# Optimization experiments

Measured on AMD Instinct MI355X. Metric: run time of the kernel, lower is better.

The kernel has to match this reference:

```python
import jax, jax.numpy as jnp
import numpy as np
import math

HEADS = 8
DIM_HEAD = 64
EMB = 512
GROUPS = 32
EPS = 100000.0  # module's literal default norm_eps


def setup_inputs() -> dict:
    key = jax.random.key(0)
    ks = jax.random.split(key, 11)
    B, D, H, W = 2, EMB, 64, 64
    s = 1.0 / math.sqrt(EMB)
    inp = {
        "input": jax.random.normal(ks[0], (B, D, H, W), dtype=jnp.float32),
        "gn_gamma": jnp.ones((EMB,), dtype=jnp.float32),
        "gn_beta": jnp.zeros((EMB,), dtype=jnp.float32),
        "wq": jax.random.normal(ks[1], (EMB, EMB), dtype=jnp.float32) * s,
        "bq": jax.random.normal(ks[2], (EMB,), dtype=jnp.float32) * 0.01,
        "wk": jax.random.normal(ks[3], (EMB, EMB), dtype=jnp.float32) * s,
        "bk": jax.random.normal(ks[4], (EMB,), dtype=jnp.float32) * 0.01,
        "wv": jax.random.normal(ks[5], (EMB, EMB), dtype=jnp.float32) * s,
        "bv": jax.random.normal(ks[6], (EMB,), dtype=jnp.float32) * 0.01,
        "wo": jax.random.normal(ks[7], (EMB, EMB), dtype=jnp.float32) * s,
        "bo": jax.random.normal(ks[8], (EMB,), dtype=jnp.float32) * 0.01,
    }
    return inp


def reference(input, gn_gamma, gn_beta, wq, bq, wk, bk, wv, bv, wo, bo):
    B, D, H, W = input.shape
    S = H * W
    residual = input

    # GroupNorm(32, D) over (C/G, H, W) per group, affine per-channel
    xg = input.reshape(B, GROUPS, (D // GROUPS) * H * W)
    mu = jnp.mean(xg, axis=-1, keepdims=True)
    var = jnp.var(xg, axis=-1, keepdims=True)
    xn = (xg - mu) / jnp.sqrt(var + EPS)
    xn = xn.reshape(B, D, H, W) * gn_gamma[:, None, None] + gn_beta[:, None, None]

    # (B, D, H, W) -> (B, S, D)
    x = xn.reshape(B, D, S).transpose(0, 2, 1)

    # projections (torch Linear: y = x @ W.T + b)
    q = (x @ wq.T + bq).reshape(B, S, HEADS, DIM_HEAD).transpose(0, 2, 1, 3)
    k = (x @ wk.T + bk).reshape(B, S, HEADS, DIM_HEAD).transpose(0, 2, 1, 3)
    v = (x @ wv.T + bv).reshape(B, S, HEADS, DIM_HEAD).transpose(0, 2, 1, 3)

    scale = 1.0 / math.sqrt(DIM_HEAD)
    scores = jnp.einsum("bhqd,bhkd->bhqk", q * scale, k)  # [B, h, S, S]
    attn = jax.nn.softmax(scores, axis=-1)
    o = jnp.einsum("bhqk,bhkd->bhqd", attn, v)  # [B, h, S, dh]
    o = o.transpose(0, 2, 1, 3).reshape(B, S, D)

    out = o @ wo.T + bo  # [B, S, D]
    out = out.transpose(0, 2, 1).reshape(B, D, H, W)
    return out + residual
```

## Files before the change

kernel.cpp:

```cpp
#include <hip/hip_runtime.h>

#define EMB 512
#define SEQ 4096
#define BATCH 2
#define NH 8
#define DH 64
#define GN_EPS 100000.0f
#define ALPHA 0.125f

typedef __bf16 bf16;
typedef __bf16 bf16x8 __attribute__((ext_vector_type(8)));
typedef float f32x4 __attribute__((ext_vector_type(4)));

typedef __attribute__((address_space(1))) unsigned int u32g;
typedef __attribute__((address_space(3))) unsigned int u32l;
__device__ __forceinline__ void gll16(const void* g, void* l) {
  __builtin_amdgcn_global_load_lds((const u32g*)g, (u32l*)l, 16, 0, 0);
}

__device__ __forceinline__ void stage8(const bf16* g, size_t rowStride, bf16* lds, int lane) {
  const int r = lane >> 3, cc = (lane & 7) ^ r;
  gll16(g + (size_t)r * rowStride + cc * 8, lds + lane * 8);
}
__device__ __forceinline__ bf16x8 frag(const bf16* lds, int r, int cc) {
  return *(const bf16x8*)&lds[(((r << 3) + (cc ^ (r & 7))) << 3)];
}

__global__ __launch_bounds__(256) void stats_k(const float* __restrict__ in,
                                               float* __restrict__ rs,
                                               float* __restrict__ ss) {
  const int row = blockIdx.x;
  const float4* p = (const float4*)(in + (size_t)row * SEQ);
  float s = 0.f, s2 = 0.f;
#pragma unroll
  for (int i = 0; i < 4; ++i) {
    float4 v = p[i * 256 + threadIdx.x];
    s += v.x + v.y + v.z + v.w;
    s2 += v.x * v.x + v.y * v.y + v.z * v.z + v.w * v.w;
  }
#pragma unroll
  for (int o = 32; o > 0; o >>= 1) {
    s += __shfl_down(s, o, 64);
    s2 += __shfl_down(s2, o, 64);
  }
  __shared__ float red[8];
  const int wave = threadIdx.x >> 6, lane = threadIdx.x & 63;
  if (lane == 0) { red[wave] = s; red[4 + wave] = s2; }
  __syncthreads();
  if (threadIdx.x == 0) {
    rs[row] = red[0] + red[1] + red[2] + red[3];
    ss[row] = red[4] + red[5] + red[6] + red[7];
  }
}

__global__ __launch_bounds__(256) void prep_k(const float* __restrict__ wq, const float* __restrict__ wk,
                                              const float* __restrict__ wv, const float* __restrict__ wo,
                                              const float* __restrict__ bv,
                                              const float* __restrict__ rs, const float* __restrict__ ss,
                                              const float* __restrict__ gamma, const float* __restrict__ beta,
                                              bf16* __restrict__ wqt, bf16* __restrict__ wkb,
                                              bf16* __restrict__ wvb, bf16* __restrict__ wob,
                                              float* __restrict__ kxa, float* __restrict__ vsuma) {
  __shared__ float t[64][65];
  __shared__ float xs[1024];
  __shared__ float gmu[64], grs[64];
  const int y = blockIdx.y, tid = threadIdx.x;
  if (y < 8) {
    const int c0 = blockIdx.x * 64, r0 = y * 64;
#pragma unroll
    for (int p = 0; p < 16; ++p) {
      int lin = p * 256 + tid;
      int rl = lin >> 6, cl = lin & 63;
      t[rl][cl] = wq[(size_t)(r0 + rl) * EMB + c0 + cl];
    }
    __syncthreads();
#pragma unroll
    for (int p = 0; p < 16; ++p) {
      int lin = p * 256 + tid;
      int cl = lin >> 6, rl = lin & 63;
      wqt[(size_t)(c0 + cl) * EMB + r0 + rl] = (bf16)t[rl][cl];
    }
  } else {
    const int wi = y - 8;
    const float* W = wi == 0 ? wk : wi == 1 ? wv : wo;
    bf16* WO = wi == 0 ? wkb : wi == 1 ? wvb : wob;
    if (wi < 2) {
      if (tid < 64) {
        float s = 0.f, s2 = 0.f;
#pragma unroll
        for (int c = 0; c < 16; ++c) { s += rs[tid * 16 + c]; s2 += ss[tid * 16 + c]; }
        float mu = s * (1.f / 65536.f);
        float var = s2 * (1.f / 65536.f) - mu * mu;
        gmu[tid] = mu;
        grs[tid] = rsqrtf(var + GN_EPS);
      }
      __syncthreads();
      for (int idx = tid; idx < 1024; idx += 256) {
        int d = idx & 511;
        float s = grs[idx >> 4] * gamma[d];
        float tt = beta[d] - gmu[idx >> 4] * s;
        xs[idx] = s * rs[idx] + 4096.f * tt;
      }
      __syncthreads();
    }
    const int n = blockIdx.x * 64 + (tid >> 2);
    const float* Wr = W + (size_t)n * EMB;
    float dot0 = 0.f, dot1 = 0.f;
    const int dq = (tid & 3) * 128;
    for (int d = dq; d < dq + 128; d += 4) {
      float4 w4 = *(const float4*)&Wr[d];
      if (wi < 2) {
        float4 x0 = *(const float4*)&xs[d];
        float4 x1 = *(const float4*)&xs[EMB + d];
        dot0 += w4.x * x0.x + w4.y * x0.y + w4.z * x0.z + w4.w * x0.w;
        dot1 += w4.x * x1.x + w4.y * x1.y + w4.z * x1.z + w4.w * x1.w;
      }
      bf16 r[4] = {(bf16)w4.x, (bf16)w4.y, (bf16)w4.z, (bf16)w4.w};
      *(uint2*)&WO[(size_t)n * EMB + d] = *(uint2*)r;
    }
    if (wi < 2) {
      dot0 += __shfl_xor(dot0, 1, 4); dot0 += __shfl_xor(dot0, 2, 4);
      dot1 += __shfl_xor(dot1, 1, 4); dot1 += __shfl_xor(dot1, 2, 4);
      if ((tid & 3) == 0) {
        if (wi == 0) { kxa[n] = dot0; kxa[EMB + n] = dot1; }
        else { vsuma[n] = dot0 + 4096.f * bv[n]; vsuma[EMB + n] = dot1 + 4096.f * bv[n]; }
      }
    }
  }
}

__global__ __launch_bounds__(256) void nx_k(const float* __restrict__ in,
                                            const float* __restrict__ rs,
                                            const float* __restrict__ ss,
                                            const float* __restrict__ gamma,
                                            const float* __restrict__ beta,
                                            bf16* __restrict__ xds,
                                            bf16* __restrict__ xsd) {
  __shared__ float t[64][65];
  __shared__ float gmu4[4], grs4[4], scl[64], ttl[64];
  const int s0 = blockIdx.x * 64, d0 = blockIdx.y * 64, b = blockIdx.z;
  const int tid = threadIdx.x;
  if (tid < 4) {
    float s = 0.f, s2 = 0.f;
    int base = b * EMB + d0 + tid * 16;
#pragma unroll
    for (int c = 0; c < 16; ++c) { s += rs[base + c]; s2 += ss[base + c]; }
    float mu = s * (1.f / 65536.f);
    float var = s2 * (1.f / 65536.f) - mu * mu;
    gmu4[tid] = mu;
    grs4[tid] = rsqrtf(var + GN_EPS);
  }
  __syncthreads();
  if (tid < 64) {
    int d = d0 + tid;
    float s = grs4[tid >> 4] * gamma[d];
    scl[tid] = s;
    ttl[tid] = beta[d] - gmu4[tid >> 4] * s;
  }
  __syncthreads();
#pragma unroll
  for (int p = 0; p < 16; ++p) {
    int lin = p * 256 + tid;
    int dl = lin >> 6, sl = lin & 63;
    size_t idx = ((size_t)b * EMB + d0 + dl) * SEQ + s0 + sl;
    float v = in[idx] * scl[dl] + ttl[dl];
    t[dl][sl] = v;
    xds[idx] = (bf16)v;
  }
  __syncthreads();
#pragma unroll
  for (int p = 0; p < 16; ++p) {
    int lin = p * 256 + tid;
    int sl = lin >> 6, dl = lin & 63;
    xsd[((size_t)b * SEQ + s0 + sl) * EMB + d0 + dl] = (bf16)t[dl][sl];
  }
}

__global__ __launch_bounds__(256) void graw2_k(const bf16* __restrict__ xds,
                                               float* __restrict__ pG) {
  __shared__ __align__(16) bf16 As[64 * 64];
  __shared__ __align__(16) bf16 Bs[64 * 64];
  int ti = 0, rem = blockIdx.x;
  while (rem >= 8 - ti) { rem -= 8 - ti; ++ti; }
  const int i0 = ti * 64, j0 = (ti + rem) * 64;
  const int kc = blockIdx.y, b = blockIdx.z;
  const bf16* X = xds + (size_t)b * EMB * SEQ;
  const int tid = threadIdx.x;
  const int wave = tid >> 6, lane = tid & 63, l16 = lane & 15, quad = lane >> 4;
  f32x4 acc[4] = {};
  for (int k0 = kc * 512; k0 < kc * 512 + 512; k0 += 64) {
#pragma unroll
    for (int p = 0; p < 2; ++p) {
      int g = wave * 2 + p;
      stage8(&X[(size_t)(i0 + g * 8) * SEQ + k0], SEQ, &As[g * 512], lane);
      stage8(&X[(size_t)(j0 + g * 8) * SEQ + k0], SEQ, &Bs[g * 512], lane);
    }
    __syncthreads();
#pragma unroll
    for (int kt = 0; kt < 2; ++kt) {
      bf16x8 af = frag(As, wave * 16 + l16, kt * 4 + quad);
#pragma unroll
      for (int nt = 0; nt < 4; ++nt) {
        bf16x8 bb = frag(Bs, nt * 16 + l16, kt * 4 + quad);
        acc[nt] = __builtin_amdgcn_mfma_f32_16x16x32_bf16(af, bb, acc[nt], 0, 0, 0);
      }
    }
    __syncthreads();
  }
  float* pg = pG + ((size_t)(b * 8 + kc) * 36 + blockIdx.x) * 4096;
#pragma unroll
  for (int nt = 0; nt < 4; ++nt)
#pragma unroll
    for (int r = 0; r < 4; ++r)
      pg[(wave * 16 + quad * 4 + r) * 64 + nt * 16 + l16] = acc[nt][r];
}

__global__ __launch_bounds__(256) void gsum_k(const float* __restrict__ pG,
                                              bf16* __restrict__ G) {
  const int b = blockIdx.x >> 10;
  const int e = ((blockIdx.x & 1023) << 8) + threadIdx.x;
  const int i = e >> 9, j = e & 511;
  int ti = i >> 6, tj = j >> 6, row = i & 63, col = j & 63;
  if (ti > tj) { int tmp = ti; ti = tj; tj = tmp; tmp = row; row = col; col = tmp; }
  const int tile = ti * 8 - (ti * (ti - 1)) / 2 + (tj - ti);
  const float* p = pG + (size_t)b * 8 * 36 * 4096 + (size_t)tile * 4096 + row * 64 + col;
  float s = 0.f;
#pragma unroll
  for (int kc = 0; kc < 8; ++kc) s += p[(size_t)kc * 36 * 4096];
  G[(size_t)b * 262144 + e] = (bf16)s;
}

__global__ __launch_bounds__(256) void t2pt_k(const bf16* __restrict__ wkb,
                                              const bf16* __restrict__ G,
                                              const bf16* __restrict__ wvb,
                                              float* __restrict__ pPt) {
  __shared__ __align__(16) bf16 As[64 * 64];
  __shared__ __align__(16) bf16 Bs[64 * 64];
  __shared__ __align__(16) bf16 Ps[4 * 16 * 72];
  const int n0 = blockIdx.x * 64, h = blockIdx.y, b = blockIdx.z;
  const int bh = b * NH + h;
  const int tid = threadIdx.x;
  const int wave = tid >> 6, lane = tid & 63, l16 = lane & 15, quad = lane >> 4;
  bf16* Pw = &Ps[wave * 16 * 72];
  f32x4 acc[4] = {};
  for (int k0 = 0; k0 < EMB; k0 += 64) {
#pragma unroll
    for (int p = 0; p < 2; ++p) {
      int g = wave * 2 + p;
      stage8(&wkb[(size_t)(h * DH + g * 8) * EMB + k0], EMB, &As[g * 512], lane);
      stage8(&G[((size_t)b * EMB + n0 + g * 8) * EMB + k0], EMB, &Bs[g * 512], lane);
    }
    __syncthreads();
#pragma unroll
    for (int kt = 0; kt < 2; ++kt) {
      bf16x8 af = frag(As, wave * 16 + l16, kt * 4 + quad);
#pragma unroll
      for (int nt = 0; nt < 4; ++nt) {
        bf16x8 bb = frag(Bs, nt * 16 + l16, kt * 4 + quad);
        acc[nt] = __builtin_amdgcn_mfma_f32_16x16x32_bf16(af, bb, acc[nt], 0, 0, 0);
      }
    }
    __syncthreads();
  }
#pragma unroll
  for (int nt = 0; nt < 4; ++nt)
#pragma unroll
    for (int r = 0; r < 4; ++r)
      Pw[(quad * 4 + r) * 72 + nt * 16 + l16] = (bf16)acc[nt][r];
#pragma unroll
  for (int p = 0; p < 2; ++p) {
    int g = wave * 2 + p;
    stage8(&wvb[(size_t)(h * DH + g * 8) * EMB + n0], EMB, &Bs[g * 512], lane);
  }
  __syncthreads();
  f32x4 accP[4] = {};
#pragma unroll
  for (int kt = 0; kt < 2; ++kt) {
    bf16x8 pf = *(const bf16x8*)&Pw[l16 * 72 + kt * 32 + quad * 8];
#pragma unroll
    for (int nt = 0; nt < 4; ++nt) {
      bf16x8 bb = frag(Bs, nt * 16 + l16, kt * 4 + quad);
      accP[nt] = __builtin_amdgcn_mfma_f32_16x16x32_bf16(pf, bb, accP[nt], 0, 0, 0);
    }
  }
  float* pp = pPt + ((size_t)bh * 8 + blockIdx.x) * 4096;
#pragma unroll
  for (int nt = 0; nt < 4; ++nt)
#pragma unroll
    for (int r = 0; r < 4; ++r)
      pp[(wave * 16 + quad * 4 + r) * 64 + nt * 16 + l16] = accP[nt][r];
}

__global__ __launch_bounds__(256) void ptsum_k(const float* __restrict__ pPt,
                                               const float* __restrict__ bk,
                                               const float* __restrict__ bv,
                                               const float* __restrict__ kxa,
                                               const float* __restrict__ vsuma,
                                               bf16* __restrict__ Pt) {
  const int bh = blockIdx.x;
  const int b = bh >> 3, h = bh & 7;
  const float sfac = ALPHA / 4096.f;
  for (int e = threadIdx.x; e < 4096; e += 256) {
    int kd = e >> 6, vd = e & 63;
    const float* p = pPt + (size_t)bh * 8 * 4096 + e;
    float s = 0.f;
#pragma unroll
    for (int nt = 0; nt < 8; ++nt) s += p[nt * 4096];
    float bvv = bv[h * DH + vd];
    float bkv = bk[h * DH + kd];
    float vx = vsuma[b * EMB + h * DH + vd] - 4096.f * bvv;
    float val = s + kxa[b * EMB + h * DH + kd] * bvv + bkv * vx + 4096.f * bkv * bvv;
    Pt[(size_t)bh * 4096 + e] = (bf16)(val * sfac);
  }
}

__global__ __launch_bounds__(256) void fchain_k(const bf16* __restrict__ wob,
                                                const bf16* __restrict__ Pt,
                                                const bf16* __restrict__ wqt,
                                                const float* __restrict__ wo,
                                                const float* __restrict__ bo,
                                                const float* __restrict__ bq,
                                                const float* __restrict__ vsuma,
                                                bf16* __restrict__ F,
                                                float* __restrict__ cst) {
  __shared__ __align__(16) bf16 Awo[64 * 64];
  __shared__ __align__(16) bf16 Bp[64 * 64];
  __shared__ __align__(16) bf16 Bwq[64 * 64];
  __shared__ __align__(16) bf16 Ps[4 * 16 * 72];
  __shared__ float yc[512];
  const int i0 = blockIdx.x * 64, j0 = blockIdx.y * 64, b = blockIdx.z;
  const int tid = threadIdx.x;
  const int wave = tid >> 6, lane = tid & 63, l16 = lane & 15, quad = lane >> 4;
  bf16* Pw = &Ps[wave * 16 * 72];
  f32x4 accF[4] = {};
  for (int h = 0; h < NH; ++h) {
    __syncthreads();
#pragma unroll
    for (int p = 0; p < 2; ++p) {
      int g = wave * 2 + p;
      stage8(&wob[(size_t)(i0 + g * 8) * EMB + h * DH], EMB, &Awo[g * 512], lane);
      stage8(&Pt[((size_t)(b * NH + h) * DH + g * 8) * DH], DH, &Bp[g * 512], lane);
      stage8(&wqt[(size_t)(j0 + g * 8) * EMB + h * DH], EMB, &Bwq[g * 512], lane);
    }
    __syncthreads();
    f32x4 at[4] = {};
#pragma unroll
    for (int kt = 0; kt < 2; ++kt) {
      bf16x8 af = frag(Awo, wave * 16 + l16, kt * 4 + quad);
#pragma unroll
      for (int nt = 0; nt < 4; ++nt) {
        bf16x8 bb = frag(Bp, nt * 16 + l16, kt * 4 + quad);
        at[nt] = __builtin_amdgcn_mfma_f32_16x16x32_bf16(af, bb, at[nt], 0, 0, 0);
      }
    }
#pragma unroll
    for (int nt = 0; nt < 4; ++nt)
#pragma unroll
      for (int r = 0; r < 4; ++r)
        Pw[(quad * 4 + r) * 72 + nt * 16 + l16] = (bf16)at[nt][r];
#pragma unroll
    for (int kt = 0; kt < 2; ++kt) {
      bf16x8 pf = *(const bf16x8*)&Pw[l16 * 72 + kt * 32 + quad * 8];
#pragma unroll
      for (int nt = 0; nt < 4; ++nt) {
        bf16x8 bb = frag(Bwq, nt * 16 + l16, kt * 4 + quad);
        accF[nt] = __builtin_amdgcn_mfma_f32_16x16x32_bf16(pf, bb, accF[nt], 0, 0, 0);
      }
    }
  }
#pragma unroll
  for (int nt = 0; nt < 4; ++nt)
#pragma unroll
    for (int r = 0; r < 4; ++r)
      F[((size_t)b * EMB + i0 + wave * 16 + quad * 4 + r) * EMB + j0 + nt * 16 + l16] =
          (bf16)accF[nt][r];
  if (j0 == 0) {
    __syncthreads();
    for (int e = tid; e < 512; e += 256) {
      int h = e >> 6, vd = e & 63;
      const bf16* pp = &Pt[(size_t)(b * NH + h) * DH * DH + vd];
      const float* bqh = &bq[h * DH];
      float a = 0.f;
#pragma unroll 8
      for (int kd = 0; kd < 64; ++kd) a += (float)pp[kd * DH] * bqh[kd];
      yc[e] = vsuma[b * EMB + e] * (1.f / 4096.f) + a;
    }
    __syncthreads();
    const int row = i0 + (tid >> 2);
    const float* wr = &wo[(size_t)row * EMB + (tid & 3) * 128];
    const float* yq = &yc[(tid & 3) * 128];
    float a = 0.f;
    for (int e = 0; e < 128; e += 4) {
      float4 w4 = *(const float4*)&wr[e];
      a += w4.x * yq[e] + w4.y * yq[e + 1] + w4.z * yq[e + 2] + w4.w * yq[e + 3];
    }
    a += __shfl_xor(a, 1, 4);
    a += __shfl_xor(a, 2, 4);
    if ((tid & 3) == 0) cst[b * EMB + row] = bo[row] + a;
  }
}

__global__ __launch_bounds__(256) void final_k(const bf16* __restrict__ F,
                                               const bf16* __restrict__ xsd,
                                               const float* __restrict__ cst,
                                               const float* __restrict__ in,
                                               float* __restrict__ out) {
  __shared__ __align__(16) bf16 As[128 * 64];
  __shared__ __align__(16) bf16 Bs[64 * 64];
  const int m0 = blockIdx.x * 128, s0 = blockIdx.y * 64, b = blockIdx.z;
  const bf16* Fb = F + (size_t)b * EMB * EMB;
  const bf16* Xb = xsd + (size_t)b * SEQ * EMB;
  const int tid = threadIdx.x;
  const int wave = tid >> 6, lane = tid & 63, l16 = lane & 15, quad = lane >> 4;
  f32x4 acc[2][4] = {};
  for (int k0 = 0; k0 < EMB; k0 += 64) {
#pragma unroll
    for (int p = 0; p < 4; ++p) {
      int g = wave * 4 + p;
      stage8(&Fb[(size_t)(m0 + g * 8) * EMB + k0], EMB, &As[g * 512], lane);
    }
#pragma unroll
    for (int p = 0; p < 2; ++p) {
      int g = wave * 2 + p;
      stage8(&Xb[(size_t)(s0 + g * 8) * EMB + k0], EMB, &Bs[g * 512], lane);
    }
    __syncthreads();
#pragma unroll
    for (int kt = 0; kt < 2; ++kt) {
      bf16x8 a0 = frag(As, wave * 32 + l16, kt * 4 + quad);
      bf16x8 a1 = frag(As, wave * 32 + 16 + l16, kt * 4 + quad);
#pragma unroll
      for (int nt = 0; nt < 4; ++nt) {
        bf16x8 bb = frag(Bs, nt * 16 + l16, kt * 4 + quad);
        acc[0][nt] = __builtin_amdgcn_mfma_f32_16x16x32_bf16(a0, bb, acc[0][nt], 0, 0, 0);
        acc[1][nt] = __builtin_amdgcn_mfma_f32_16x16x32_bf16(a1, bb, acc[1][nt], 0, 0, 0);
      }
    }
    __syncthreads();
  }
#pragma unroll
  for (int mt = 0; mt < 2; ++mt) {
    int rowl = m0 + wave * 32 + mt * 16 + quad * 4;
#pragma unroll
    for (int r = 0; r < 4; ++r) {
      float cv = cst[b * EMB + rowl + r];
      size_t base = ((size_t)b * EMB + rowl + r) * SEQ + s0;
#pragma unroll
      for (int nt = 0; nt < 4; ++nt) {
        size_t idx = base + nt * 16 + l16;
        out[idx] = in[idx] + cv + acc[mt][nt][r];
      }
    }
  }
}

extern "C" void kernel_launch(void* const* d_in, const int* in_sizes, int n_in,
                              void* d_out, int out_size, void* d_ws, size_t ws_size,
                              hipStream_t stream) {
  const float* inp = (const float*)d_in[0];
  const float* gam = (const float*)d_in[1];
  const float* bet = (const float*)d_in[2];
  const float* wq = (const float*)d_in[3];
  const float* bq = (const float*)d_in[4];
  const float* wk = (const float*)d_in[5];
  const float* bk = (const float*)d_in[6];
  const float* wv = (const float*)d_in[7];
  const float* bv = (const float*)d_in[8];
  const float* wo = (const float*)d_in[9];
  const float* bo = (const float*)d_in[10];
  float* out = (float*)d_out;
  (void)in_sizes; (void)n_in; (void)out_size; (void)ws_size;

  char* ws = (char*)d_ws;
  size_t off = 0;
  auto take = [&](size_t bytes) -> char* {
    char* p = ws + off;
    off += (bytes + 255) & ~(size_t)255;
    return p;
  };
  float* rs = (float*)take(1024 * 4);
  float* ssq = (float*)take(1024 * 4);
  float* kxa = (float*)take(1024 * 4);
  float* vsuma = (float*)take(1024 * 4);
  float* cst = (float*)take(1024 * 4);
  const size_t WB = (size_t)EMB * EMB * sizeof(bf16);
  bf16* wkb = (bf16*)take(WB);
  bf16* wvb = (bf16*)take(WB);
  bf16* wob = (bf16*)take(WB);
  bf16* wqtb = (bf16*)take(WB);
  const size_t XB = (size_t)BATCH * SEQ * EMB * sizeof(bf16);
  bf16* xds = (bf16*)take(XB);
  bf16* xsd = (bf16*)take(XB);
  float* pG = (float*)take((size_t)BATCH * 8 * 36 * 4096 * sizeof(float));
  bf16* G = (bf16*)take((size_t)BATCH * EMB * EMB * sizeof(bf16));
  float* pPt = (float*)take((size_t)16 * 8 * 4096 * sizeof(float));
  bf16* Pt = (bf16*)take((size_t)16 * 4096 * sizeof(bf16));
  bf16* F = (bf16*)take((size_t)BATCH * EMB * EMB * sizeof(bf16));

  stats_k<<<1024, 256, 0, stream>>>(inp, rs, ssq);
  prep_k<<<dim3(8, 11), 256, 0, stream>>>(wq, wk, wv, wo, bv, rs, ssq, gam, bet,
                                          wqtb, wkb, wvb, wob, kxa, vsuma);
  nx_k<<<dim3(64, 8, 2), 256, 0, stream>>>(inp, rs, ssq, gam, bet, xds, xsd);
  graw2_k<<<dim3(36, 8, 2), 256, 0, stream>>>(xds, pG);
  gsum_k<<<2048, 256, 0, stream>>>(pG, G);
  t2pt_k<<<dim3(8, 8, 2), 256, 0, stream>>>(wkb, G, wvb, pPt);
  ptsum_k<<<16, 256, 0, stream>>>(pPt, bk, bv, kxa, vsuma, Pt);
  fchain_k<<<dim3(8, 8, 2), 256, 0, stream>>>(wob, Pt, wqtb, wo, bo, bq, vsuma, F, cst);
  final_k<<<dim3(4, 64, 2), 256, 0, stream>>>(F, xsd, cst, inp, out);
}
```

Before: 177.3 us.

## Fuse prep and normalize kernels, double split-K, split fchain into two GEMMs

Merges the weight-prep and normalize/transpose kernels into a single launch so their blocks run concurrently. It doubles the split-K factor in the Gram and t2pt GEMMs to put more blocks on the device, at the cost of larger partial buffers and reduction work. The serial per-head chain in fchain is split into a per-head Y kernel (with atomic accumulation of the constant term) and a plain GEMM. The bias-vector precompute moves into ptsum. This raises parallelism in the small late stages but adds one launch and an intermediate Y buffer round-trip.

```diff
diff --git a/kernel.cpp b/kernel.cpp
--- a/kernel.cpp
+++ b/kernel.cpp
@@ -53,126 +53,122 @@
   }
 }
 
-__global__ __launch_bounds__(256) void prep_k(const float* __restrict__ wq, const float* __restrict__ wk,
-                                              const float* __restrict__ wv, const float* __restrict__ wo,
-                                              const float* __restrict__ bv,
-                                              const float* __restrict__ rs, const float* __restrict__ ss,
-                                              const float* __restrict__ gamma, const float* __restrict__ beta,
-                                              bf16* __restrict__ wqt, bf16* __restrict__ wkb,
-                                              bf16* __restrict__ wvb, bf16* __restrict__ wob,
-                                              float* __restrict__ kxa, float* __restrict__ vsuma) {
+__global__ __launch_bounds__(256) void nxprep_k(const float* __restrict__ in,
+                                                const float* __restrict__ rs, const float* __restrict__ ss,
+                                                const float* __restrict__ gamma, const float* __restrict__ beta,
+                                                const float* __restrict__ wq, const float* __restrict__ wk,
+                                                const float* __restrict__ wv, const float* __restrict__ wo,
+                                                const float* __restrict__ bv,
+                                                bf16* __restrict__ xds, bf16* __restrict__ xsd,
+                                                bf16* __restrict__ wqt, bf16* __restrict__ wkb,
+                                                bf16* __restrict__ wvb, bf16* __restrict__ wob,
+                                                float* __restrict__ kxa, float* __restrict__ vsuma) {
   __shared__ float t[64][65];
   __shared__ float xs[1024];
   __shared__ float gmu[64], grs[64];
-  const int y = blockIdx.y, tid = threadIdx.x;
-  if (y < 8) {
-    const int c0 = blockIdx.x * 64, r0 = y * 64;
+  const int id = blockIdx.x, tid = threadIdx.x;
+  if (id < 1024) {
+    const int b = id >> 9, rem = id & 511;
+    const int d0 = (rem >> 6) * 64, s0 = (rem & 63) * 64;
+    if (tid < 4) {
+      float s = 0.f, s2 = 0.f;
+      int base = b * EMB + d0 + tid * 16;
+#pragma unroll
+      for (int c = 0; c < 16; ++c) { s += rs[base + c]; s2 += ss[base + c]; }
+      float mu = s * (1.f / 65536.f);
+      float var = s2 * (1.f / 65536.f) - mu * mu;
+      gmu[tid] = mu;
+      grs[tid] = rsqrtf(var + GN_EPS);
+    }
+    __syncthreads();
+    if (tid < 64) {
+      int d = d0 + tid;
+      float s = grs[tid >> 4] * gamma[d];
+      xs[tid] = s;
+      xs[64 + tid] = beta[d] - gmu[tid >> 4] * s;
+    }
+    __syncthreads();
 #pragma unroll
     for (int p = 0; p < 16; ++p) {
       int lin = p * 256 + tid;
-      int rl = lin >> 6, cl = lin & 63;
-      t[rl][cl] = wq[(size_t)(r0 + rl) * EMB + c0 + cl];
+      int dl = lin >> 6, sl = lin & 63;
+      size_t idx = ((size_t)b * EMB + d0 + dl) * SEQ + s0 + sl;
+      float v = in[idx] * xs[dl] + xs[64 + dl];
+      t[dl][sl] = v;
+      xds[idx] = (bf16)v;
     }
     __syncthreads();
 #pragma unroll
     for (int p = 0; p < 16; ++p) {
       int lin = p * 256 + tid;
-      int cl = lin >> 6, rl = lin & 63;
-      wqt[(size_t)(c0 + cl) * EMB + r0 + rl] = (bf16)t[rl][cl];
+      int sl = lin >> 6, dl = lin & 63;
+      xsd[((size_t)b * SEQ + s0 + sl) * EMB + d0 + dl] = (bf16)t[dl][sl];
     }
   } else {
-    const int wi = y - 8;
-    const float* W = wi == 0 ? wk : wi == 1 ? wv : wo;
-    bf16* WO = wi == 0 ? wkb : wi == 1 ? wvb : wob;
-    if (wi < 2) {
-      if (tid < 64) {
-        float s = 0.f, s2 = 0.f;
-#pragma unroll
-        for (int c = 0; c < 16; ++c) { s += rs[tid * 16 + c]; s2 += ss[tid * 16 + c]; }
-        float mu = s * (1.f / 65536.f);
-        float var = s2 * (1.f / 65536.f) - mu * mu;
-        gmu[tid] = mu;
-        grs[tid] = rsqrtf(var + GN_EPS);
+    const int r = id - 1024;
+    const int bx = r & 7, y = r >> 3;
+    if (y < 8) {
+      const int c0 = bx * 64, r0 = y * 64;
+#pragma unroll
+      for (int p = 0; p < 16; ++p) {
+        int lin = p * 256 + tid;
+        int rl = lin >> 6, cl = lin & 63;
+        t[rl][cl] = wq[(size_t)(r0 + rl) * EMB + c0 + cl];
       }
       __syncthreads();
-      for (int idx = tid; idx < 1024; idx += 256) {
-        int d = idx & 511;
-        float s = grs[idx >> 4] * gamma[d];
-        float tt = beta[d] - gmu[idx >> 4] * s;
-        xs[idx] = s * rs[idx] + 4096.f * tt;
-      }
-      __syncthreads();
-    }
-    const int n = blockIdx.x * 64 + (tid >> 2);
-    const float* Wr = W + (size_t)n * EMB;
-    float dot0 = 0.f, dot1 = 0.f;
-    const int dq = (tid & 3) * 128;
-    for (int d = dq; d < dq + 128; d += 4) {
-      float4 w4 = *(const float4*)&Wr[d];
+#pragma unroll
+      for (int p = 0; p < 16; ++p) {
+        int lin = p * 256 + tid;
+        int cl = lin >> 6, rl = lin & 63;
+        wqt[(size_t)(c0 + cl) * EMB + r0 + rl] = (bf16)t[rl][cl];
+      }
+    } else {
+      const int wi = y - 8;
+      const float* W = wi == 0 ? wk : wi == 1 ? wv : wo;
+      bf16* WO = wi == 0 ? wkb : wi == 1 ? wvb : wob;
       if (wi < 2) {
-        float4 x0 = *(const float4*)&xs[d];
-        float4 x1 = *(const float4*)&xs[EMB + d];
-        dot0 += w4.x * x0.x + w4.y * x0.y + w4.z * x0.z + w4.w * x0.w;
-        dot1 += w4.x * x1.x + w4.y * x1.y + w4.z * x1.z + w4.w * x1.w;
-      }
-      bf16 r[4] = {(bf16)w4.x, (bf16)w4.y, (bf16)w4.z, (bf16)w4.w};
-      *(uint2*)&WO[(size_t)n * EMB + d] = *(uint2*)r;
-    }
-    if (wi < 2) {
-      dot0 += __shfl_xor(dot0, 1, 4); dot0 += __shfl_xor(dot0, 2, 4);
-      dot1 += __shfl_xor(dot1, 1, 4); dot1 += __shfl_xor(dot1, 2, 4);
-      if ((tid & 3) == 0) {
-        if (wi == 0) { kxa[n] = dot0; kxa[EMB + n] = dot1; }
-        else { vsuma[n] = dot0 + 4096.f * bv[n]; vsuma[EMB + n] = dot1 + 4096.f * bv[n]; }
-      }
-    }
-  }
-}
-
-__global__ __launch_bounds__(256) void nx_k(const float* __restrict__ in,
-                                            const float* __restrict__ rs,
-                                            const float* __restrict__ ss,
-                                            const float* __restrict__ gamma,
-                                            const float* __restrict__ beta,
-                                            bf16* __restrict__ xds,
-                                            bf16* __restrict__ xsd) {
-  __shared__ float t[64][65];
-  __shared__ float gmu4[4], grs4[4], scl[64], ttl[64];
-  const int s0 = blockIdx.x * 64, d0 = blockIdx.y * 64, b = blockIdx.z;
-  const int tid = threadIdx.x;
-  if (tid < 4) {
-    float s = 0.f, s2 = 0.f;
-    int base = b * EMB + d0 + tid * 16;
-#pragma unroll
-    for (int c = 0; c < 16; ++c) { s += rs[base + c]; s2 += ss[base + c]; }
-    float mu = s * (1.f / 65536.f);
-    float var = s2 * (1.f / 65536.f) - mu * mu;
-    gmu4[tid] = mu;
-    grs4[tid] = rsqrtf(var + GN_EPS);
-  }
-  __syncthreads();
-  if (tid < 64) {
-    int d = d0 + tid;
-    float s = grs4[tid >> 4] * gamma[d];
-    scl[tid] = s;
-    ttl[tid] = beta[d] - gmu4[tid >> 4] * s;
-  }
-  __syncthreads();
-#pragma unroll
-  for (int p = 0; p < 16; ++p) {
-    int lin = p * 256 + tid;
-    int dl = lin >> 6, sl = lin & 63;
-    size_t idx = ((size_t)b * EMB + d0 + dl) * SEQ + s0 + sl;
-    float v = in[idx] * scl[dl] + ttl[dl];
-    t[dl][sl] = v;
-    xds[idx] = (bf16)v;
-  }
-  __syncthreads();
-#pragma unroll
-  for (int p = 0; p < 16; ++p) {
-    int lin = p * 256 + tid;
-    int sl = lin >> 6, dl = lin & 63;
-    xsd[((size_t)b * SEQ + s0 + sl) * EMB + d0 + dl] = (bf16)t[dl][sl];
+        if (tid < 64) {
+          float s = 0.f, s2 = 0.f;
+#pragma unroll
+          for (int c = 0; c < 16; ++c) { s += rs[tid * 16 + c]; s2 += ss[tid * 16 + c]; }
+          float mu = s * (1.f / 65536.f);
+          float var = s2 * (1.f / 65536.f) - mu * mu;
+          gmu[tid] = mu;
+          grs[tid] = rsqrtf(var + GN_EPS);
+        }
+        __syncthreads();
+        for (int idx = tid; idx < 1024; idx += 256) {
+          int d = idx & 511;
+          float s = grs[idx >> 4] * gamma[d];
+          float tt = beta[d] - gmu[idx >> 4] * s;
+          xs[idx] = s * rs[idx] + 4096.f * tt;
+        }
+        __syncthreads();
+      }
+      const int n = bx * 64 + (tid >> 2);
+      const float* Wr = W + (size_t)n * EMB;
+      float dot0 = 0.f, dot1 = 0.f;
+      const int dq = (tid & 3) * 128;
+      for (int d = dq; d < dq + 128; d += 4) {
+        float4 w4 = *(const float4*)&Wr[d];
+        if (wi < 2) {
+          float4 x0 = *(const float4*)&xs[d];
+          float4 x1 = *(const float4*)&xs[EMB + d];
+          dot0 += w4.x * x0.x + w4.y * x0.y + w4.z * x0.z + w4.w * x0.w;
+          dot1 += w4.x * x1.x + w4.y * x1.y + w4.z * x1.z + w4.w * x1.w;
+        }
+        bf16 rr[4] = {(bf16)w4.x, (bf16)w4.y, (bf16)w4.z, (bf16)w4.w};
+        *(uint2*)&WO[(size_t)n * EMB + d] = *(uint2*)rr;
+      }
+      if (wi < 2) {
+        dot0 += __shfl_xor(dot0, 1, 4); dot0 += __shfl_xor(dot0, 2, 4);
+        dot1 += __shfl_xor(dot1, 1, 4); dot1 += __shfl_xor(dot1, 2, 4);
+        if ((tid & 3) == 0) {
+          if (wi == 0) { kxa[n] = dot0; kxa[EMB + n] = dot1; }
+          else { vsuma[n] = dot0 + 4096.f * bv[n]; vsuma[EMB + n] = dot1 + 4096.f * bv[n]; }
+        }
+      }
+    }
   }
 }
 
@@ -188,7 +184,7 @@
   const int tid = threadIdx.x;
   const int wave = tid >> 6, lane = tid & 63, l16 = lane & 15, quad = lane >> 4;
   f32x4 acc[4] = {};
-  for (int k0 = kc * 512; k0 < kc * 512 + 512; k0 += 64) {
+  for (int k0 = kc * 256; k0 < kc * 256 + 256; k0 += 64) {
 #pragma unroll
     for (int p = 0; p < 2; ++p) {
       int g = wave * 2 + p;
@@ -207,7 +203,7 @@
     }
     __syncthreads();
   }
-  float* pg = pG + ((size_t)(b * 8 + kc) * 36 + blockIdx.x) * 4096;
+  float* pg = pG + ((size_t)(b * 16 + kc) * 36 + blockIdx.x) * 4096;
 #pragma unroll
   for (int nt = 0; nt < 4; ++nt)
 #pragma unroll
@@ -223,10 +219,10 @@
   int ti = i >> 6, tj = j >> 6, row = i & 63, col = j & 63;
   if (ti > tj) { int tmp = ti; ti = tj; tj = tmp; tmp = row; row = col; col = tmp; }
   const int tile = ti * 8 - (ti * (ti - 1)) / 2 + (tj - ti);
-  const float* p = pG + (size_t)b * 8 * 36 * 4096 + (size_t)tile * 4096 + row * 64 + col;
+  const float* p = pG + (size_t)b * 16 * 36 * 4096 + (size_t)tile * 4096 + row * 64 + col;
   float s = 0.f;
 #pragma unroll
-  for (int kc = 0; kc < 8; ++kc) s += p[(size_t)kc * 36 * 4096];
+  for (int kc = 0; kc < 16; ++kc) s += p[(size_t)kc * 36 * 4096];
   G[(size_t)b * 262144 + e] = (bf16)s;
 }
 
@@ -237,13 +233,14 @@
   __shared__ __align__(16) bf16 As[64 * 64];
   __shared__ __align__(16) bf16 Bs[64 * 64];
   __shared__ __align__(16) bf16 Ps[4 * 16 * 72];
-  const int n0 = blockIdx.x * 64, h = blockIdx.y, b = blockIdx.z;
+  const int n0 = blockIdx.x * 64, h = blockIdx.y;
+  const int b = blockIdx.z & 1, kc = blockIdx.z >> 1;
   const int bh = b * NH + h;
   const int tid = threadIdx.x;
   const int wave = tid >> 6, lane = tid & 63, l16 = lane & 15, quad = lane >> 4;
   bf16* Pw = &Ps[wave * 16 * 72];
   f32x4 acc[4] = {};
-  for (int k0 = 0; k0 < EMB; k0 += 64) {
+  for (int k0 = kc * 256; k0 < kc * 256 + 256; k0 += 64) {
 #pragma unroll
     for (int p = 0; p < 2; ++p) {
       int g = wave * 2 + p;
@@ -283,7 +280,7 @@
       accP[nt] = __builtin_amdgcn_mfma_f32_16x16x32_bf16(pf, bb, accP[nt], 0, 0, 0);
     }
   }
-  float* pp = pPt + ((size_t)bh * 8 + blockIdx.x) * 4096;
+  float* pp = pPt + ((size_t)bh * 16 + blockIdx.x * 2 + kc) * 4096;
 #pragma unroll
   for (int nt = 0; nt < 4; ++nt)
 #pragma unroll
@@ -296,108 +293,128 @@
                                                const float* __restrict__ bv,
                                                const float* __restrict__ kxa,
                                                const float* __restrict__ vsuma,
-                                               bf16* __restrict__ Pt) {
+                                               const float* __restrict__ bq,
+                                               const float* __restrict__ bo,
+                                               bf16* __restrict__ Pt,
+                                               float* __restrict__ ycat,
+                                               float* __restrict__ cst) {
+  __shared__ bf16 ptl[4096];
   const int bh = blockIdx.x;
   const int b = bh >> 3, h = bh & 7;
   const float sfac = ALPHA / 4096.f;
-  for (int e = threadIdx.x; e < 4096; e += 256) {
+  const int tid = threadIdx.x;
+  for (int e = tid; e < 4096; e += 256) {
     int kd = e >> 6, vd = e & 63;
-    const float* p = pPt + (size_t)bh * 8 * 4096 + e;
+    const float* p = pPt + (size_t)bh * 16 * 4096 + e;
     float s = 0.f;
 #pragma unroll
-    for (int nt = 0; nt < 8; ++nt) s += p[nt * 4096];
+    for (int nt = 0; nt < 16; ++nt) s += p[nt * 4096];
     float bvv = bv[h * DH + vd];
     float bkv = bk[h * DH + kd];
     float vx = vsuma[b * EMB + h * DH + vd] - 4096.f * bvv;
     float val = s + kxa[b * EMB + h * DH + kd] * bvv + bkv * vx + 4096.f * bkv * bvv;
-    Pt[(size_t)bh * 4096 + e] = (bf16)(val * sfac);
-  }
-}
-
-__global__ __launch_bounds__(256) void fchain_k(const bf16* __restrict__ wob,
-                                                const bf16* __restrict__ Pt,
-                                                const bf16* __restrict__ wqt,
-                                                const float* __restrict__ wo,
-                                                const float* __restrict__ bo,
-                                                const float* __restrict__ bq,
-                                                const float* __restrict__ vsuma,
-                                                bf16* __restrict__ F,
-                                                float* __restrict__ cst) {
-  __shared__ __align__(16) bf16 Awo[64 * 64];
+    bf16 pv = (bf16)(val * sfac);
+    Pt[(size_t)bh * 4096 + e] = pv;
+    ptl[e] = pv;
+  }
+  __syncthreads();
+  if (tid < 64) {
+    float a = 0.f;
+    const float* bqh = &bq[h * DH];
+#pragma unroll 8
+    for (int kd = 0; kd < 64; ++kd) a += (float)ptl[kd * 64 + tid] * bqh[kd];
+    ycat[b * EMB + h * DH + tid] = vsuma[b * EMB + h * DH + tid] * (1.f / 4096.f) + a;
+  }
+  if (h == 0) {
+    for (int i = tid; i < EMB; i += 256) cst[b * EMB + i] = bo[i];
+  }
+}
+
+__global__ __launch_bounds__(256) void yk_k(const bf16* __restrict__ wob,
+                                            const bf16* __restrict__ Pt,
+                                            const float* __restrict__ wo,
+                                            const float* __restrict__ ycat,
+                                            bf16* __restrict__ Y,
+                                            float* __restrict__ cst) {
+  __shared__ __align__(16) bf16 Aw[64 * 64];
   __shared__ __align__(16) bf16 Bp[64 * 64];
-  __shared__ __align__(16) bf16 Bwq[64 * 64];
-  __shared__ __align__(16) bf16 Ps[4 * 16 * 72];
-  __shared__ float yc[512];
+  __shared__ float ycl[64];
+  const int i0 = blockIdx.x * 64, h = blockIdx.y, b = blockIdx.z;
+  const int bh = b * NH + h;
+  const int tid = threadIdx.x;
+  const int wave = tid >> 6, lane = tid & 63, l16 = lane & 15, quad = lane >> 4;
+#pragma unroll
+  for (int p = 0; p < 2; ++p) {
+    int g = wave * 2 + p;
+    stage8(&wob[(size_t)(i0 + g * 8) * EMB + h * DH], EMB, &Aw[g * 512], lane);
+    stage8(&Pt[(size_t)bh * 4096 + (g * 8) * 64], 64, &Bp[g * 512], lane);
+  }
+  if (tid < 64) ycl[tid] = ycat[b * EMB + h * DH + tid];
+  __syncthreads();
+  f32x4 acc[4] = {};
+#pragma unroll
+  for (int kt = 0; kt < 2; ++kt) {
+    bf16x8 af = frag(Aw, wave * 16 + l16, kt * 4 + quad);
+#pragma unroll
+    for (int nt = 0; nt < 4; ++nt) {
+      bf16x8 bb = frag(Bp, nt * 16 + l16, kt * 4 + quad);
+      acc[nt] = __builtin_amdgcn_mfma_f32_16x16x32_bf16(af, bb, acc[nt], 0, 0, 0);
+    }
+  }
+#pragma unroll
+  for (int nt = 0; nt < 4; ++nt)
+#pragma unroll
+    for (int r = 0; r < 4; ++r)
+      Y[((size_t)b * EMB + i0 + wave * 16 + quad * 4 + r) * EMB + h * DH + nt * 16 + l16] =
+          (bf16)acc[nt][r];
+  const int row = i0 + (tid >> 2);
+  const float* wr = &wo[(size_t)row * EMB + h * DH + (tid & 3) * 16];
+  const float* yq = &ycl[(tid & 3) * 16];
+  float a = 0.f;
+#pragma unroll
+  for (int e = 0; e < 16; e += 4) {
+    float4 w4 = *(const float4*)&wr[e];
+    a += w4.x * yq[e] + w4.y * yq[e + 1] + w4.z * yq[e + 2] + w4.w * yq[e + 3];
+  }
+  a += __shfl_xor(a, 1, 4);
+  a += __shfl_xor(a, 2, 4);
+  if ((tid & 3) == 0) atomicAdd(&cst[b * EMB + row], a);
+}
+
+__global__ __launch_bounds__(256) void fgemm_k(const bf16* __restrict__ Y,
+                                               const bf16* __restrict__ wqt,
+                                               bf16* __restrict__ F) {
+  __shared__ __align__(16) bf16 As[64 * 64];
+  __shared__ __align__(16) bf16 Bs[64 * 64];
   const int i0 = blockIdx.x * 64, j0 = blockIdx.y * 64, b = blockIdx.z;
   const int tid = threadIdx.x;
   const int wave = tid >> 6, lane = tid & 63, l16 = lane & 15, quad = lane >> 4;
-  bf16* Pw = &Ps[wave * 16 * 72];
-  f32x4 accF[4] = {};
-  for (int h = 0; h < NH; ++h) {
-    __syncthreads();
+  f32x4 acc[4] = {};
+  for (int k0 = 0; k0 < EMB; k0 += 64) {
 #pragma unroll
     for (int p = 0; p < 2; ++p) {
       int g = wave * 2 + p;
-      stage8(&wob[(size_t)(i0 + g * 8) * EMB + h * DH], EMB, &Awo[g * 512], lane);
-      stage8(&Pt[((size_t)(b * NH + h) * DH + g * 8) * DH], DH, &Bp[g * 512], lane);
-      stage8(&wqt[(size_t)(j0 + g * 8) * EMB + h * DH], EMB, &Bwq[g * 512], lane);
-    }
-    __syncthreads();
-    f32x4 at[4] = {};
+      stage8(&Y[((size_t)b * EMB + i0 + g * 8) * EMB + k0], EMB, &As[g * 512], lane);
+      stage8(&wqt[(size_t)(j0 + g * 8) * EMB + k0], EMB, &Bs[g * 512], lane);
+    }
+    __syncthreads();
 #pragma unroll
     for (int kt = 0; kt < 2; ++kt) {
-      bf16x8 af = frag(Awo, wave * 16 + l16, kt * 4 + quad);
+      bf16x8 af = frag(As, wave * 16 + l16, kt * 4 + quad);
 #pragma unroll
       for (int nt = 0; nt < 4; ++nt) {
-        bf16x8 bb = frag(Bp, nt * 16 + l16, kt * 4 + quad);
-        at[nt] = __builtin_amdgcn_mfma_f32_16x16x32_bf16(af, bb, at[nt], 0, 0, 0);
-      }
-    }
-#pragma unroll
-    for (int nt = 0; nt < 4; ++nt)
-#pragma unroll
-      for (int r = 0; r < 4; ++r)
-        Pw[(quad * 4 + r) * 72 + nt * 16 + l16] = (bf16)at[nt][r];
-#pragma unroll
-    for (int kt = 0; kt < 2; ++kt) {
-      bf16x8 pf = *(const bf16x8*)&Pw[l16 * 72 + kt * 32 + quad * 8];
-#pragma unroll
-      for (int nt = 0; nt < 4; ++nt) {
-        bf16x8 bb = frag(Bwq, nt * 16 + l16, kt * 4 + quad);
-        accF[nt] = __builtin_amdgcn_mfma_f32_16x16x32_bf16(pf, bb, accF[nt], 0, 0, 0);
-      }
-    }
+        bf16x8 bb = frag(Bs, nt * 16 + l16, kt * 4 + quad);
+        acc[nt] = __builtin_amdgcn_mfma_f32_16x16x32_bf16(af, bb, acc[nt], 0, 0, 0);
+      }
+    }
+    __syncthreads();
   }
 #pragma unroll
   for (int nt = 0; nt < 4; ++nt)
 #pragma unroll
     for (int r = 0; r < 4; ++r)
       F[((size_t)b * EMB + i0 + wave * 16 + quad * 4 + r) * EMB + j0 + nt * 16 + l16] =
-          (bf16)accF[nt][r];
-  if (j0 == 0) {
-    __syncthreads();
-    for (int e = tid; e < 512; e += 256) {
-      int h = e >> 6, vd = e & 63;
-      const bf16* pp = &Pt[(size_t)(b * NH + h) * DH * DH + vd];
-      const float* bqh = &bq[h * DH];
-      float a = 0.f;
-#pragma unroll 8
-      for (int kd = 0; kd < 64; ++kd) a += (float)pp[kd * DH] * bqh[kd];
-      yc[e] = vsuma[b * EMB + e] * (1.f / 4096.f) + a;
-    }
-    __syncthreads();
-    const int row = i0 + (tid >> 2);
-    const float* wr = &wo[(size_t)row * EMB + (tid & 3) * 128];
-    const float* yq = &yc[(tid & 3) * 128];
-    float a = 0.f;
-    for (int e = 0; e < 128; e += 4) {
-      float4 w4 = *(const float4*)&wr[e];
-      a += w4.x * yq[e] + w4.y * yq[e + 1] + w4.z * yq[e + 2] + w4.w * yq[e + 3];
-    }
-    a += __shfl_xor(a, 1, 4);
-    a += __shfl_xor(a, 2, 4);
-    if ((tid & 3) == 0) cst[b * EMB + row] = bo[row] + a;
-  }
+          (bf16)acc[nt][r];
 }
 
 __global__ __launch_bounds__(256) void final_k(const bf16* __restrict__ F,
@@ -483,6 +500,7 @@
   float* kxa = (float*)take(1024 * 4);
   float* vsuma = (float*)take(1024 * 4);
   float* cst = (float*)take(1024 * 4);
+  float* ycat = (float*)take(1024 * 4);
   const size_t WB = (size_t)EMB * EMB * sizeof(bf16);
   bf16* wkb = (bf16*)take(WB);
   bf16* wvb = (bf16*)take(WB);
@@ -491,20 +509,21 @@
   const size_t XB = (size_t)BATCH * SEQ * EMB * sizeof(bf16);
   bf16* xds = (bf16*)take(XB);
   bf16* xsd = (bf16*)take(XB);
-  float* pG = (float*)take((size_t)BATCH * 8 * 36 * 4096 * sizeof(float));
+  float* pG = (float*)take((size_t)BATCH * 16 * 36 * 4096 * sizeof(float));
   bf16* G = (bf16*)take((size_t)BATCH * EMB * EMB * sizeof(bf16));
-  float* pPt = (float*)take((size_t)16 * 8 * 4096 * sizeof(float));
+  float* pPt = (float*)take((size_t)16 * 16 * 4096 * sizeof(float));
   bf16* Pt = (bf16*)take((size_t)16 * 4096 * sizeof(bf16));
+  bf16* Y = (bf16*)take((size_t)BATCH * EMB * EMB * sizeof(bf16));
   bf16* F = (bf16*)take((size_t)BATCH * EMB * EMB * sizeof(bf16));
 
   stats_k<<<1024, 256, 0, stream>>>(inp, rs, ssq);
-  prep_k<<<dim3(8, 11), 256, 0, stream>>>(wq, wk, wv, wo, bv, rs, ssq, gam, bet,
-                                          wqtb, wkb, wvb, wob, kxa, vsuma);
-  nx_k<<<dim3(64, 8, 2), 256, 0, stream>>>(inp, rs, ssq, gam, bet, xds, xsd);
-  graw2_k<<<dim3(36, 8, 2), 256, 0, stream>>>(xds, pG);
+  nxprep_k<<<1112, 256, 0, stream>>>(inp, rs, ssq, gam, bet, wq, wk, wv, wo, bv,
+                                     xds, xsd, wqtb, wkb, wvb, wob, kxa, vsuma);
+  graw2_k<<<dim3(36, 16, 2), 256, 0, stream>>>(xds, pG);
   gsum_k<<<2048, 256, 0, stream>>>(pG, G);
-  t2pt_k<<<dim3(8, 8, 2), 256, 0, stream>>>(wkb, G, wvb, pPt);
-  ptsum_k<<<16, 256, 0, stream>>>(pPt, bk, bv, kxa, vsuma, Pt);
-  fchain_k<<<dim3(8, 8, 2), 256, 0, stream>>>(wob, Pt, wqtb, wo, bo, bq, vsuma, F, cst);
+  t2pt_k<<<dim3(8, 8, 4), 256, 0, stream>>>(wkb, G, wvb, pPt);
+  ptsum_k<<<16, 256, 0, stream>>>(pPt, bk, bv, kxa, vsuma, bq, bo, Pt, ycat, cst);
+  yk_k<<<dim3(8, 8, 2), 256, 0, stream>>>(wob, Pt, wo, ycat, Y, cst);
+  fgemm_k<<<dim3(8, 8, 2), 256, 0, stream>>>(Y, wqtb, F);
   final_k<<<dim3(4, 64, 2), 256, 0, stream>>>(F, xsd, cst, inp, out);
 }
```

Measured after the change: 181.7 us. 1.02x slower.
